# Performance work log

Measured on AMD Instinct MI355X. Metric: run time of the kernel, lower is better.

## Reference

```python
import jax, jax.numpy as jnp
import numpy as np


def setup_inputs() -> dict:
    key = jax.random.key(0)
    k1, k2, k3, k4 = jax.random.split(key, 4)
    B, T, D, U = 32, 2048, 256, 256
    x = jax.random.normal(k1, (B, T, D), dtype=jnp.float32)
    Wz = jax.random.normal(k2, (D + U, U), dtype=jnp.float32) * 0.05
    Wr = jax.random.normal(k3, (D + U, U), dtype=jnp.float32) * 0.05
    Wh = jax.random.normal(k4, (D + U, U), dtype=jnp.float32) * 0.05
    return {"x": x, "Wz": Wz, "Wr": Wr, "Wh": Wh}


def reference(x, Wz, Wr, Wh):
    # GRU recurrence: z = sigmoid([x,h] Wz); r = sigmoid([x,h] Wr);
    # h_hat = tanh([x, r*h] Wh); h' = z*h + (1-z)*h_hat
    B = x.shape[0]
    U = Wz.shape[1]
    h0 = jnp.zeros((B, U), dtype=x.dtype)

    def step(h, x_t):
        x_h = jnp.concatenate([x_t, h], axis=-1)          # [B, D+U]
        z = jax.nn.sigmoid(x_h @ Wz)                       # [B, U]
        r = jax.nn.sigmoid(x_h @ Wr)                       # [B, U]
        x_rh = jnp.concatenate([x_t, r * h], axis=-1)      # [B, D+U]
        h_hat = jnp.tanh(x_rh @ Wh)                        # [B, U]
        new_h = z * h + (1.0 - z) * h_hat
        return new_h, new_h

    xs = jnp.swapaxes(x, 0, 1)                             # [T, B, D]
    _, ys = jax.lax.scan(step, h0, xs)                     # ys: [T, B, U]
    return jnp.swapaxes(ys, 0, 1)                          # [B, T, U]
```

## Files before the change

### kernel.cpp

```cpp
#include <hip/hip_runtime.h>
#include <hip/hip_fp16.h>
#include <stdint.h>

#define NB 32
#define NT 2048
#define ND 256
#define NU 256

typedef _Float16 f16x2 __attribute__((ext_vector_type(2)));

__device__ __forceinline__ float fdot2u(uint32_t a, uint32_t b, float c) {
#if __has_builtin(__builtin_amdgcn_fdot2)
  return __builtin_amdgcn_fdot2(__builtin_bit_cast(f16x2, a),
                                __builtin_bit_cast(f16x2, b), c, false);
#else
  f16x2 av = __builtin_bit_cast(f16x2, a);
  f16x2 bv = __builtin_bit_cast(f16x2, b);
  return c + (float)av.x * (float)bv.x + (float)av.y * (float)bv.y;
#endif
}

__device__ __forceinline__ uint32_t packh2(float lo, float hi) {
  f16x2 p;
  p.x = (_Float16)lo;
  p.y = (_Float16)hi;
  return __builtin_bit_cast(uint32_t, p);
}

struct SRec {
  float hbuf[NU];
  alignas(16) uint32_t h2[NU / 2];
  alignas(16) uint32_t rh2[NU / 2];
  float psz[2][NU];
  float psr[2][NU];
  float psh[2][NU];
};
struct SGemm {
  float a[64][132];
  float b[64][68];
};

__global__ __launch_bounds__(512) void gru_combined(
    const float* __restrict__ x, const float* __restrict__ Wz,
    const float* __restrict__ Wr, const float* __restrict__ Wh,
    const uint32_t* __restrict__ Wf16, float* __restrict__ hstate,
    float* __restrict__ out, const float* __restrict__ Gsrc,
    float* __restrict__ Gdst, int t0r, int t0g, int recCnt, int chunkT) {
  __shared__ union SM {
    SRec r;
    SGemm g;
  } sm;
  const int tid = threadIdx.x;

  if ((int)blockIdx.x < recCnt) {
    const int b = blockIdx.x;
    const int u = tid & (NU - 1);
    const int kh = tid >> 8;

    uint4 wzv[16], wrv[16], whv[16];
    const uint4* W4 = (const uint4*)Wf16;
    const int wb = u * 32 + kh * 16;
#pragma unroll
    for (int j = 0; j < 16; j++) wzv[j] = W4[(0 * NU) * 32 + wb + j];
#pragma unroll
    for (int j = 0; j < 16; j++) wrv[j] = W4[(1 * NU) * 32 + wb + j];
#pragma unroll
    for (int j = 0; j < 16; j++) whv[j] = W4[(2 * NU) * 32 + wb + j];

    if (tid < NU) sm.r.hbuf[tid] = hstate[b * NU + tid];
    __syncthreads();
    if (tid < NU / 2) sm.r.h2[tid] = packh2(sm.r.hbuf[2 * tid], sm.r.hbuf[2 * tid + 1]);
    __syncthreads();

    float z = 0.f, r = 0.f, hu = 0.f;
    for (int tt = 0; tt < chunkT; ++tt) {
      float gz = 0.f, gr = 0.f, gh = 0.f;
      if (tid < NU) {
        const float* Gp = Gsrc + (size_t)(tt * 3) * NB * NU + b * NU + u;
        gz = Gp[0];
        gr = Gp[NB * NU];
        gh = Gp[2 * NB * NU];
      }
      float az = 0.f, ar = 0.f;
#pragma unroll
      for (int jb = 0; jb < 16; jb++) {
        uint4 hv = *(const uint4*)&sm.r.h2[(kh * 16 + jb) * 4];
        az = fdot2u(wzv[jb].x, hv.x, az);
        az = fdot2u(wzv[jb].y, hv.y, az);
        az = fdot2u(wzv[jb].z, hv.z, az);
        az = fdot2u(wzv[jb].w, hv.w, az);
        ar = fdot2u(wrv[jb].x, hv.x, ar);
        ar = fdot2u(wrv[jb].y, hv.y, ar);
        ar = fdot2u(wrv[jb].z, hv.z, ar);
        ar = fdot2u(wrv[jb].w, hv.w, ar);
      }
      sm.r.psz[kh][u] = az;
      sm.r.psr[kh][u] = ar;
      __syncthreads();
      if (tid < NU) {
        float sz = gz + sm.r.psz[0][u] + sm.r.psz[1][u];
        float sr = gr + sm.r.psr[0][u] + sm.r.psr[1][u];
        z = 1.f / (1.f + __expf(-sz));
        r = 1.f / (1.f + __expf(-sr));
        hu = sm.r.hbuf[u];
        float rh = r * hu;
        float rh1 = __shfl_down(rh, 1);
        if ((u & 1) == 0) sm.r.rh2[u >> 1] = packh2(rh, rh1);
      }
      __syncthreads();
      float ah = 0.f;
#pragma unroll
      for (int jb = 0; jb < 16; jb++) {
        uint4 rv = *(const uint4*)&sm.r.rh2[(kh * 16 + jb) * 4];
        ah = fdot2u(whv[jb].x, rv.x, ah);
        ah = fdot2u(whv[jb].y, rv.y, ah);
        ah = fdot2u(whv[jb].z, rv.z, ah);
        ah = fdot2u(whv[jb].w, rv.w, ah);
      }
      sm.r.psh[kh][u] = ah;
      __syncthreads();
      if (tid < NU) {
        float hh = tanhf(gh + sm.r.psh[0][u] + sm.r.psh[1][u]);
        float hn = z * hu + (1.f - z) * hh;
        sm.r.hbuf[u] = hn;
        out[((size_t)b * NT + (t0r + tt)) * NU + u] = hn;
        float hn1 = __shfl_down(hn, 1);
        if ((u & 1) == 0) sm.r.h2[u >> 1] = packh2(hn, hn1);
      }
      __syncthreads();
    }
    if (tid < NU) hstate[b * NU + tid] = sm.r.hbuf[tid];

  } else if (Gdst != nullptr) {
    const int gg = (int)blockIdx.x - recCnt;
    const int mtile = gg / 12;
    const int ntile = gg - mtile * 12;
    const int g = ntile >> 2;
    const int u0 = (ntile & 3) * 64;
    const float* Wg = (g == 0) ? Wz : ((g == 1) ? Wr : Wh);
    const int ty = tid >> 4;
    const int tx = tid & 15;
    const int mbase = mtile * 128;
    float acc[4][4] = {{0.f}};

    for (int kk = 0; kk < 4; ++kk) {
      const int k0 = kk * 64;
      __syncthreads();
      {
        const int ml = tid & 127;
        const int kq = tid >> 7;
        const int m = mbase + ml;
        const int bb = m / chunkT;
        const int tt = m - bb * chunkT;
        const float* xp = x + ((size_t)bb * NT + t0g + tt) * ND + k0 + kq * 16;
#pragma unroll
        for (int v = 0; v < 4; ++v) {
          float4 xv = ((const float4*)xp)[v];
          sm.g.a[kq * 16 + v * 4 + 0][ml] = xv.x;
          sm.g.a[kq * 16 + v * 4 + 1][ml] = xv.y;
          sm.g.a[kq * 16 + v * 4 + 2][ml] = xv.z;
          sm.g.a[kq * 16 + v * 4 + 3][ml] = xv.w;
        }
      }
      {
        const int nl = (tid & 15) * 4;
        const int kr = tid >> 4;
#pragma unroll
        for (int s = 0; s < 2; ++s) {
          const int krow = kr + s * 32;
          float4 wv = *(const float4*)&Wg[(size_t)(k0 + krow) * NU + u0 + nl];
          *(float4*)&sm.g.b[krow][nl] = wv;
        }
      }
      __syncthreads();
#pragma unroll 8
      for (int k = 0; k < 64; ++k) {
        const float4 av = *(const float4*)&sm.g.a[k][ty * 4];
        const float4 bv = *(const float4*)&sm.g.b[k][tx * 4];
        acc[0][0] += av.x * bv.x; acc[0][1] += av.x * bv.y; acc[0][2] += av.x * bv.z; acc[0][3] += av.x * bv.w;
        acc[1][0] += av.y * bv.x; acc[1][1] += av.y * bv.y; acc[1][2] += av.y * bv.z; acc[1][3] += av.y * bv.w;
        acc[2][0] += av.z * bv.x; acc[2][1] += av.z * bv.y; acc[2][2] += av.z * bv.z; acc[2][3] += av.z * bv.w;
        acc[3][0] += av.w * bv.x; acc[3][1] += av.w * bv.y; acc[3][2] += av.w * bv.z; acc[3][3] += av.w * bv.w;
      }
    }
#pragma unroll
    for (int i = 0; i < 4; ++i) {
      const int m = mbase + ty * 4 + i;
      const int bb = m / chunkT;
      const int tt = m - bb * chunkT;
      float4 val;
      val.x = acc[i][0]; val.y = acc[i][1]; val.z = acc[i][2]; val.w = acc[i][3];
      *(float4*)&Gdst[((size_t)(tt * 3 + g) * NB + bb) * NU + u0 + tx * 4] = val;
    }
  }
}

__global__ void gru_prep(const float* __restrict__ Wz, const float* __restrict__ Wr,
                         const float* __restrict__ Wh, uint32_t* __restrict__ Wf16,
                         float* __restrict__ hstate) {
  const int idx = blockIdx.x * 256 + threadIdx.x;
  const int NW = 3 * NU * 128;
  if (idx < NW) {
    const int g = idx / (NU * 128);
    const int rem = idx - g * (NU * 128);
    const int u = rem >> 7;
    const int p = rem & 127;
    const float* Wg = (g == 0) ? Wz : ((g == 1) ? Wr : Wh);
    float w0 = Wg[(size_t)(ND + 2 * p) * NU + u];
    float w1 = Wg[(size_t)(ND + 2 * p + 1) * NU + u];
    Wf16[idx] = packh2(w0, w1);
  } else {
    const int j = idx - NW;
    if (j < NB * NU) hstate[j] = 0.f;
  }
}

extern "C" void kernel_launch(void* const* d_in, const int* in_sizes, int n_in,
                              void* d_out, int out_size, void* d_ws, size_t ws_size,
                              hipStream_t stream) {
  (void)in_sizes; (void)n_in; (void)out_size;
  const float* x = (const float*)d_in[0];
  const float* Wz = (const float*)d_in[1];
  const float* Wr = (const float*)d_in[2];
  const float* Wh = (const float*)d_in[3];
  float* out = (float*)d_out;

  int ct = 8;
  const int cands[6] = {256, 128, 64, 32, 16, 8};
  for (int i = 0; i < 6; ++i) {
    size_t need = 2ull * cands[i] * 3 * NB * NU * 4 + (1u << 20);
    if (need <= ws_size) { ct = cands[i]; break; }
  }
  const int nch = NT / ct;
  const size_t chunkBytes = (size_t)ct * 3 * NB * NU * 4;

  char* wsb = (char*)d_ws;
  float* G0 = (float*)wsb;
  float* G1 = (float*)(wsb + chunkBytes);
  uint32_t* Wf16 = (uint32_t*)(wsb + 2 * chunkBytes);
  float* hstate = (float*)(wsb + 2 * chunkBytes + (size_t)3 * NU * 128 * 4);

  const int prepThreads = 3 * NU * 128 + NB * NU;
  gru_prep<<<(prepThreads + 255) / 256, 256, 0, stream>>>(Wz, Wr, Wh, Wf16, hstate);

  gru_combined<<<3 * ct, 512, 0, stream>>>(x, Wz, Wr, Wh, Wf16, hstate, out,
                                           nullptr, G0, 0, 0, 0, ct);
  for (int k = 0; k < nch; ++k) {
    float* Gsrc = (k & 1) ? G1 : G0;
    float* Gdst = (k & 1) ? G0 : G1;
    const int gemmOn = (k + 1 < nch) ? 1 : 0;
    gru_combined<<<32 + (gemmOn ? 3 * ct : 0), 512, 0, stream>>>(
        x, Wz, Wr, Wh, Wf16, hstate, out, Gsrc, gemmOn ? Gdst : nullptr,
        k * ct, (k + 1) * ct, 32, ct);
  }
}
```

Baseline: 3.116 ms.

## Split z and r gates across thread halves to remove a barrier per step

The recurrent block now gives each half of the 512 threads a whole gate: threads 0-255 compute the full z dot product and threads 256-511 compute the full r dot product, each over all of K. This removes the shared-memory partial-sum exchange and one __syncthreads per timestep, leaving three barriers per step instead of four. The change also uses fast rcp-based sigmoid and tanh, four independent accumulators to break the fdot2 dependency chains, and a waves_per_eu(2,2) attribute to allow more registers. Each thread now holds 48 uint4 weight registers, so register pressure rises and spills are a risk. The fast tanh also costs some accuracy.

New measurement: 2.908 ms. -6.7%, faster.

```diff
diff --git a/kernel.cpp b/kernel.cpp
--- a/kernel.cpp
+++ b/kernel.cpp
@@ -27,20 +27,28 @@
   return __builtin_bit_cast(uint32_t, p);
 }
 
+__device__ __forceinline__ float rcp_fast(float x) { return __builtin_amdgcn_rcpf(x); }
+__device__ __forceinline__ float sigmoid_fast(float x) {
+  return rcp_fast(1.f + __expf(-x));
+}
+__device__ __forceinline__ float tanh_fast(float x) {
+  return 1.f - 2.f * rcp_fast(1.f + __expf(2.f * x));
+}
+
 struct SRec {
   float hbuf[NU];
   alignas(16) uint32_t h2[NU / 2];
   alignas(16) uint32_t rh2[NU / 2];
-  float psz[2][NU];
-  float psr[2][NU];
-  float psh[2][NU];
+  float psh[NU];
 };
 struct SGemm {
   float a[64][132];
   float b[64][68];
 };
 
-__global__ __launch_bounds__(512) void gru_combined(
+__global__ __launch_bounds__(512)
+__attribute__((amdgpu_waves_per_eu(2, 2)))
+void gru_combined(
     const float* __restrict__ x, const float* __restrict__ Wz,
     const float* __restrict__ Wr, const float* __restrict__ Wh,
     const uint32_t* __restrict__ Wf16, float* __restrict__ hstate,
@@ -55,81 +63,86 @@
   if ((int)blockIdx.x < recCnt) {
     const int b = blockIdx.x;
     const int u = tid & (NU - 1);
-    const int kh = tid >> 8;
-
-    uint4 wzv[16], wrv[16], whv[16];
+    const int role = tid >> 8;
+
+    uint4 wfull[32], wh[16];
     const uint4* W4 = (const uint4*)Wf16;
-    const int wb = u * 32 + kh * 16;
-#pragma unroll
-    for (int j = 0; j < 16; j++) wzv[j] = W4[(0 * NU) * 32 + wb + j];
-#pragma unroll
-    for (int j = 0; j < 16; j++) wrv[j] = W4[(1 * NU) * 32 + wb + j];
-#pragma unroll
-    for (int j = 0; j < 16; j++) whv[j] = W4[(2 * NU) * 32 + wb + j];
-
-    if (tid < NU) sm.r.hbuf[tid] = hstate[b * NU + tid];
+    const int baseFull = role * (NU * 32) + u * 32;
+#pragma unroll
+    for (int j = 0; j < 32; j++) wfull[j] = W4[baseFull + j];
+    const int baseH = 2 * (NU * 32) + u * 32 + role * 16;
+#pragma unroll
+    for (int j = 0; j < 16; j++) wh[j] = W4[baseH + j];
+
+    float hu = 0.f;
+    if (tid < NU) {
+      hu = hstate[b * NU + tid];
+      sm.r.hbuf[tid] = hu;
+    }
     __syncthreads();
     if (tid < NU / 2) sm.r.h2[tid] = packh2(sm.r.hbuf[2 * tid], sm.r.hbuf[2 * tid + 1]);
     __syncthreads();
 
-    float z = 0.f, r = 0.f, hu = 0.f;
+    const float* Gb = Gsrc + (size_t)b * NU + u;
+    float* outp = out + ((size_t)b * NT + t0r) * NU + u;
+
     for (int tt = 0; tt < chunkT; ++tt) {
-      float gz = 0.f, gr = 0.f, gh = 0.f;
-      if (tid < NU) {
-        const float* Gp = Gsrc + (size_t)(tt * 3) * NB * NU + b * NU + u;
-        gz = Gp[0];
-        gr = Gp[NB * NU];
-        gh = Gp[2 * NB * NU];
-      }
-      float az = 0.f, ar = 0.f;
+      float g0, g1 = 0.f;
+      {
+        const float* Gt = Gb + (size_t)(tt * 3) * NB * NU;
+        if (role == 0) {
+          g0 = Gt[0];
+          g1 = Gt[2 * NB * NU];
+        } else {
+          g0 = Gt[NB * NU];
+        }
+      }
+      float a0 = 0.f, a1 = 0.f, a2 = 0.f, a3 = 0.f;
+#pragma unroll
+      for (int jb = 0; jb < 32; jb++) {
+        uint4 hv = *(const uint4*)&sm.r.h2[jb * 4];
+        a0 = fdot2u(wfull[jb].x, hv.x, a0);
+        a1 = fdot2u(wfull[jb].y, hv.y, a1);
+        a2 = fdot2u(wfull[jb].z, hv.z, a2);
+        a3 = fdot2u(wfull[jb].w, hv.w, a3);
+      }
+      const float ssum = ((a0 + a1) + (a2 + a3)) + g0;
+      float zval = 0.f;
+      if (role == 1) {
+        const float rr = sigmoid_fast(ssum);
+        const float hprev = sm.r.hbuf[u];
+        const float rh = rr * hprev;
+        const float rh1 = __shfl_down(rh, 1);
+        if ((u & 1) == 0) sm.r.rh2[u >> 1] = packh2(rh, rh1);
+      } else {
+        zval = sigmoid_fast(ssum);
+      }
+      __syncthreads();
+      float c0 = 0.f, c1 = 0.f, c2 = 0.f, c3 = 0.f;
 #pragma unroll
       for (int jb = 0; jb < 16; jb++) {
-        uint4 hv = *(const uint4*)&sm.r.h2[(kh * 16 + jb) * 4];
-        az = fdot2u(wzv[jb].x, hv.x, az);
-        az = fdot2u(wzv[jb].y, hv.y, az);
-        az = fdot2u(wzv[jb].z, hv.z, az);
-        az = fdot2u(wzv[jb].w, hv.w, az);
-        ar = fdot2u(wrv[jb].x, hv.x, ar);
-        ar = fdot2u(wrv[jb].y, hv.y, ar);
-        ar = fdot2u(wrv[jb].z, hv.z, ar);
-        ar = fdot2u(wrv[jb].w, hv.w, ar);
-      }
-      sm.r.psz[kh][u] = az;
-      sm.r.psr[kh][u] = ar;
-      __syncthreads();
-      if (tid < NU) {
-        float sz = gz + sm.r.psz[0][u] + sm.r.psz[1][u];
-        float sr = gr + sm.r.psr[0][u] + sm.r.psr[1][u];
-        z = 1.f / (1.f + __expf(-sz));
-        r = 1.f / (1.f + __expf(-sr));
-        hu = sm.r.hbuf[u];
-        float rh = r * hu;
-        float rh1 = __shfl_down(rh, 1);
-        if ((u & 1) == 0) sm.r.rh2[u >> 1] = packh2(rh, rh1);
-      }
-      __syncthreads();
-      float ah = 0.f;
-#pragma unroll
-      for (int jb = 0; jb < 16; jb++) {
-        uint4 rv = *(const uint4*)&sm.r.rh2[(kh * 16 + jb) * 4];
-        ah = fdot2u(whv[jb].x, rv.x, ah);
-        ah = fdot2u(whv[jb].y, rv.y, ah);
-        ah = fdot2u(whv[jb].z, rv.z, ah);
-        ah = fdot2u(whv[jb].w, rv.w, ah);
-      }
-      sm.r.psh[kh][u] = ah;
-      __syncthreads();
-      if (tid < NU) {
-        float hh = tanhf(gh + sm.r.psh[0][u] + sm.r.psh[1][u]);
-        float hn = z * hu + (1.f - z) * hh;
+        uint4 rv = *(const uint4*)&sm.r.rh2[(role * 16 + jb) * 4];
+        c0 = fdot2u(wh[jb].x, rv.x, c0);
+        c1 = fdot2u(wh[jb].y, rv.y, c1);
+        c2 = fdot2u(wh[jb].z, rv.z, c2);
+        c3 = fdot2u(wh[jb].w, rv.w, c3);
+      }
+      const float csum = (c0 + c1) + (c2 + c3);
+      if (role == 1) sm.r.psh[u] = csum;
+      __syncthreads();
+      if (role == 0) {
+        const float hh = tanh_fast(g1 + csum + sm.r.psh[u]);
+        const float hn = zval * hu + (1.f - zval) * hh;
+        hu = hn;
+        outp[0] = hn;
         sm.r.hbuf[u] = hn;
-        out[((size_t)b * NT + (t0r + tt)) * NU + u] = hn;
-        float hn1 = __shfl_down(hn, 1);
+        const float hn1 = __shfl_down(hn, 1);
         if ((u & 1) == 0) sm.r.h2[u >> 1] = packh2(hn, hn1);
       }
-      __syncthreads();
-    }
-    if (tid < NU) hstate[b * NU + tid] = sm.r.hbuf[tid];
+      outp += NU;
+      __syncthreads();
+    }
+    if (role == 0) hstate[b * NU + u] = hu;
 
   } else if (Gdst != nullptr) {
     const int gg = (int)blockIdx.x - recCnt;
```
